# Kernel tuning notes

Hardware: AMD Instinct MI355X
Metric: run time of the kernel (lower is better)

Reference implementation:

```python
import jax, jax.numpy as jnp
import numpy as np

E, CAP, S, H, I, K = 160, 120, 3200, 2048, 192, 6  # experts, capacity, seq, hidden, per-device ffn dim, top-k


def setup_inputs() -> dict:
    key = jax.random.key(0)
    ks = jax.random.split(key, 8)
    hidden_states = jax.random.normal(ks[0], (S, H), jnp.float32)
    token_index = jax.random.randint(ks[1], (E, CAP), 0, S, dtype=jnp.int32)
    # re_index is a permutation mapping concatenated per-expert outputs back to (topk, seq) order
    re_index = jax.random.permutation(ks[2], E * CAP).astype(jnp.int32)
    topk_weight = jax.random.uniform(ks[3], (K, S, 1), jnp.float32)
    shared_out = jax.random.normal(ks[4], (1, S, H), jnp.float32)
    scale = 0.02
    gate_w = jax.random.normal(ks[5], (E, I, H), jnp.float32) * scale
    up_w = jax.random.normal(ks[6], (E, I, H), jnp.float32) * scale
    down_w = jax.random.normal(ks[7], (E, H, I), jnp.float32) * scale
    return {
        "hidden_states": hidden_states,
        "token_index": token_index,
        "re_index": re_index,
        "topk_weight": topk_weight,
        "shared_out": shared_out,
        "gate_w": gate_w,
        "up_w": up_w,
        "down_w": down_w,
    }


def reference(hidden_states, token_index, re_index, topk_weight, shared_out, gate_w, up_w, down_w):
    # Gather per-expert token groups: [E, CAP, H]
    x = hidden_states[token_index]
    # SwiGLU expert FFN, batched over all experts (grouped GEMM)
    g = jnp.einsum('ech,eih->eci', x, gate_w)   # [E, CAP, I]
    u = jnp.einsum('ech,eih->eci', x, up_w)     # [E, CAP, I]
    h = jax.nn.silu(g) * u
    o = jnp.einsum('eci,ehi->ech', h, down_w)   # [E, CAP, H]
    # Scatter back into (topk, seq) layout and combine with routing weights
    flat = o.reshape(E * CAP, H)[re_index].reshape(K, S, H)
    out = (flat * topk_weight).sum(axis=0, keepdims=True) + shared_out  # [1, S, H]
    return out
```

## Files before the change

### kernel.cpp

```cpp
#include <hip/hip_runtime.h>
#include <hip/hip_bf16.h>

#define E_ 160
#define CAP_ 120
#define S_ 3200
#define H_ 2048
#define I_ 192
#define K_ 6
#define MP_ 128

typedef __attribute__((ext_vector_type(8))) short short8;
typedef __attribute__((ext_vector_type(4))) float f32x4;

__device__ __forceinline__ unsigned pack2bf(float a, float b) {
  return __builtin_amdgcn_perm(__float_as_uint(b), __float_as_uint(a), 0x07060302u);
}
__device__ __forceinline__ short f2bf1(float a) {
  return (short)(__float_as_uint(a) >> 16);
}
__device__ __forceinline__ float bf2f(short s) {
  return __uint_as_float(((unsigned)(unsigned short)s) << 16);
}

__global__ __launch_bounds__(256) void k_gather(
    const float* __restrict__ hidden, const int* __restrict__ tok,
    short* __restrict__ xb)
{
  int b = blockIdx.x;
  int e = b >> 7, c = b & 127;
  int col = threadIdx.x * 8;
  short* dst = xb + (size_t)b * H_ + col;
  if (c < CAP_) {
    int row = tok[e * CAP_ + c];
    const float* src = hidden + (size_t)row * H_ + col;
    float4 f0 = *(const float4*)src;
    float4 f1 = *(const float4*)(src + 4);
    int4 v;
    v.x = (int)pack2bf(f0.x, f0.y); v.y = (int)pack2bf(f0.z, f0.w);
    v.z = (int)pack2bf(f1.x, f1.y); v.w = (int)pack2bf(f1.z, f1.w);
    *(int4*)dst = v;
  } else {
    *(int4*)dst = make_int4(0, 0, 0, 0);
  }
}

__global__ __launch_bounds__(256) void k_gateup(
    const short* __restrict__ xb, const float* __restrict__ gw,
    const float* __restrict__ uw, short* __restrict__ hb)
{
  __shared__ __align__(16) char smem[34816];
  short* As = (short*)smem;
  short* Bs = As + 128 * 64;

  int bid = blockIdx.x;
  int e = bid / 3, t = bid - e * 3;
  int i0 = t * 64;
  int tid = threadIdx.x;
  int lane = tid & 63, w = tid >> 6;
  int wr = w >> 1, wc = w & 1;
  int lrow = lane & 15, lq = lane >> 4;

  f32x4 acc[4][4] = {};
  const size_t xbase = (size_t)e * MP_ * H_;

  for (int kk = 0; kk < H_ / 64; ++kk) {
    int k0 = kk * 64;
#pragma unroll
    for (int r = 0; r < 4; ++r) {
      int q = r * 256 + tid;
      int row = q >> 3, cc = q & 7;
      int4 v = *(const int4*)(xb + xbase + (size_t)row * H_ + k0 + cc * 8);
      *(int4*)(As + row * 64 + cc * 8) = v;
    }
#pragma unroll
    for (int r = 0; r < 8; ++r) {
      int p = r * 256 + tid;
      int row = p >> 4, cc = p & 15;
      const float* srcw = (row < 64)
          ? (gw + ((size_t)e * I_ + i0 + row) * H_ + k0 + cc * 4)
          : (uw + ((size_t)e * I_ + i0 + row - 64) * H_ + k0 + cc * 4);
      float4 f = *(const float4*)srcw;
      uint2 pv;
      pv.x = pack2bf(f.x, f.y); pv.y = pack2bf(f.z, f.w);
      *(uint2*)(Bs + row * 64 + cc * 4) = pv;
    }
    __syncthreads();
#pragma unroll
    for (int ks = 0; ks < 2; ++ks) {
      int koff = ks * 32 + lq * 8;
      short8 a[4], bb[4];
#pragma unroll
      for (int tr = 0; tr < 4; ++tr)
        a[tr] = *(const short8*)(As + (wr * 64 + tr * 16 + lrow) * 64 + koff);
#pragma unroll
      for (int tc = 0; tc < 4; ++tc)
        bb[tc] = *(const short8*)(Bs + (wc * 64 + tc * 16 + lrow) * 64 + koff);
#pragma unroll
      for (int tr = 0; tr < 4; ++tr)
#pragma unroll
        for (int tc = 0; tc < 4; ++tc)
          acc[tr][tc] = __builtin_amdgcn_mfma_f32_16x16x32_bf16(
              a[tr], bb[tc], acc[tr][tc], 0, 0, 0);
    }
    __syncthreads();
  }

  float* exch = (float*)smem;
  if (wc == 0) {
#pragma unroll
    for (int tr = 0; tr < 4; ++tr)
#pragma unroll
      for (int tc = 0; tc < 4; ++tc)
#pragma unroll
        for (int rg = 0; rg < 4; ++rg) {
          int lr = tr * 16 + lq * 4 + rg;
          int lcol = tc * 16 + lrow;
          exch[(wr * 64 + lr) * 68 + lcol] = acc[tr][tc][rg];
        }
  }
  __syncthreads();
  if (wc == 1) {
#pragma unroll
    for (int tr = 0; tr < 4; ++tr)
#pragma unroll
      for (int tc = 0; tc < 4; ++tc)
#pragma unroll
        for (int rg = 0; rg < 4; ++rg) {
          int lr = tr * 16 + lq * 4 + rg;
          int lcol = tc * 16 + lrow;
          float g = exch[(wr * 64 + lr) * 68 + lcol];
          float u = acc[tr][tc][rg];
          float hv = g / (1.f + __expf(-g)) * u;
          hb[((size_t)e * MP_ + wr * 64 + lr) * I_ + i0 + lcol] = f2bf1(hv);
        }
  }
}

__global__ __launch_bounds__(256) void k_down(
    const short* __restrict__ hb, const float* __restrict__ dw,
    short* __restrict__ ob)
{
  __shared__ __align__(16) short As[128 * 64];
  __shared__ __align__(16) short Bs[128 * 64];
  int bid = blockIdx.x;
  int e = bid >> 4, t = bid & 15;
  int n0 = t * 128;
  int tid = threadIdx.x;
  int lane = tid & 63, w = tid >> 6;
  int wr = w >> 1, wc = w & 1;
  int lrow = lane & 15, lq = lane >> 4;

  f32x4 acc[4][4] = {};

  for (int kk = 0; kk < 3; ++kk) {
    int k0 = kk * 64;
#pragma unroll
    for (int r = 0; r < 4; ++r) {
      int q = r * 256 + tid;
      int row = q >> 3, cc = q & 7;
      int4 v = *(const int4*)(hb + ((size_t)e * MP_ + row) * I_ + k0 + cc * 8);
      *(int4*)(As + row * 64 + cc * 8) = v;
    }
#pragma unroll
    for (int r = 0; r < 8; ++r) {
      int p = r * 256 + tid;
      int row = p >> 4, cc = p & 15;
      const float* srcw = dw + ((size_t)e * H_ + n0 + row) * I_ + k0 + cc * 4;
      float4 f = *(const float4*)srcw;
      uint2 pv;
      pv.x = pack2bf(f.x, f.y); pv.y = pack2bf(f.z, f.w);
      *(uint2*)(Bs + row * 64 + cc * 4) = pv;
    }
    __syncthreads();
#pragma unroll
    for (int ks = 0; ks < 2; ++ks) {
      int koff = ks * 32 + lq * 8;
      short8 a[4], bb[4];
#pragma unroll
      for (int tr = 0; tr < 4; ++tr)
        a[tr] = *(const short8*)(As + (wr * 64 + tr * 16 + lrow) * 64 + koff);
#pragma unroll
      for (int tc = 0; tc < 4; ++tc)
        bb[tc] = *(const short8*)(Bs + (wc * 64 + tc * 16 + lrow) * 64 + koff);
#pragma unroll
      for (int tr = 0; tr < 4; ++tr)
#pragma unroll
        for (int tc = 0; tc < 4; ++tc)
          acc[tr][tc] = __builtin_amdgcn_mfma_f32_16x16x32_bf16(
              a[tr], bb[tc], acc[tr][tc], 0, 0, 0);
    }
    __syncthreads();
  }

#pragma unroll
  for (int tr = 0; tr < 4; ++tr) {
#pragma unroll
    for (int rg = 0; rg < 4; ++rg) {
      int c = wr * 64 + tr * 16 + lq * 4 + rg;
      if (c < CAP_) {
#pragma unroll
        for (int tc = 0; tc < 4; ++tc) {
          int col = n0 + wc * 64 + tc * 16 + lrow;
          ob[((size_t)e * CAP_ + c) * H_ + col] = f2bf1(acc[tr][tc][rg]);
        }
      }
    }
  }
}

__global__ __launch_bounds__(256) void k_combine(
    const short* __restrict__ ob, const int* __restrict__ re_index,
    const float* __restrict__ topk, const float* __restrict__ shared_out,
    float* __restrict__ out)
{
  int s = blockIdx.x;
  int c0 = threadIdx.x * 8;
  const float* sh = shared_out + (size_t)s * H_ + c0;
  float4 s0 = *(const float4*)sh;
  float4 s1 = *(const float4*)(sh + 4);
  float r[8] = {s0.x, s0.y, s0.z, s0.w, s1.x, s1.y, s1.z, s1.w};
#pragma unroll
  for (int k = 0; k < K_; ++k) {
    int p = k * S_ + s;
    int idx = re_index[p];
    float wgt = topk[p];
    const short* row = ob + (size_t)idx * H_ + c0;
    short8 v = *(const short8*)row;
#pragma unroll
    for (int j = 0; j < 8; ++j) r[j] += wgt * bf2f(v[j]);
  }
  float* o = out + (size_t)s * H_ + c0;
  float4 o0, o1;
  o0.x = r[0]; o0.y = r[1]; o0.z = r[2]; o0.w = r[3];
  o1.x = r[4]; o1.y = r[5]; o1.z = r[6]; o1.w = r[7];
  *(float4*)o = o0;
  *(float4*)(o + 4) = o1;
}

extern "C" void kernel_launch(void* const* d_in, const int* in_sizes, int n_in,
                              void* d_out, int out_size, void* d_ws, size_t ws_size,
                              hipStream_t stream) {
  const float* hidden     = (const float*)d_in[0];
  const int*   tok        = (const int*)d_in[1];
  const int*   re_index   = (const int*)d_in[2];
  const float* topk       = (const float*)d_in[3];
  const float* shared_out = (const float*)d_in[4];
  const float* gw         = (const float*)d_in[5];
  const float* uw         = (const float*)d_in[6];
  const float* dw         = (const float*)d_in[7];
  float* out = (float*)d_out;

  char* ws = (char*)d_ws;
  short* xb = (short*)ws;
  short* hb = (short*)(ws + (size_t)E_ * MP_ * H_ * 2);
  short* ob = (short*)(ws + (size_t)E_ * MP_ * H_ * 2
                          + (size_t)E_ * MP_ * I_ * 2);

  hipLaunchKernelGGL(k_gather,  dim3(E_ * MP_), dim3(256), 0, stream, hidden, tok, xb);
  hipLaunchKernelGGL(k_gateup,  dim3(E_ * 3),   dim3(256), 0, stream, xb, gw, uw, hb);
  hipLaunchKernelGGL(k_down,    dim3(E_ * 16),  dim3(256), 0, stream, hb, dw, ob);
  hipLaunchKernelGGL(k_combine, dim3(S_),       dim3(256), 0, stream, ob, re_index, topk, shared_out, out);
}
```

Measured before the change: 755.5 us.

## Fuse token gather into gate/up GEMM with register prefetch and swizzled LDS

Removes the separate gather kernel and loads hidden rows directly by token index inside the gate/up GEMM, converting to bf16 on the fly. The gate/up main loop now double-buffers LDS with register prefetch of the next K slice, using one barrier per iteration and raised wave priority around the MFMAs. Both GEMMs use an XOR-swizzled LDS layout to cut bank conflicts and remap block IDs so neighbouring blocks land on the same XCD. This saves the intermediate bf16 activation round trip through memory. In exchange it adds register pressure, and the gate/up kernel now requests 64KB of shared memory with a launch bound of 2 blocks per CU.

New measurement: 706.7 us. -6.5%, faster.

```diff
diff --git a/kernel.cpp b/kernel.cpp
--- a/kernel.cpp
+++ b/kernel.cpp
@@ -21,89 +21,112 @@
 __device__ __forceinline__ float bf2f(short s) {
   return __uint_as_float(((unsigned)(unsigned short)s) << 16);
 }
-
-__global__ __launch_bounds__(256) void k_gather(
+__device__ __forceinline__ int swz(int row, int inrow_byte) {
+  return row * 128 + (inrow_byte ^ ((row & 7) << 4));
+}
+
+__global__ __launch_bounds__(256, 2) void k_gateup(
     const float* __restrict__ hidden, const int* __restrict__ tok,
-    short* __restrict__ xb)
+    const float* __restrict__ gw, const float* __restrict__ uw,
+    short* __restrict__ hb)
 {
-  int b = blockIdx.x;
-  int e = b >> 7, c = b & 127;
-  int col = threadIdx.x * 8;
-  short* dst = xb + (size_t)b * H_ + col;
-  if (c < CAP_) {
-    int row = tok[e * CAP_ + c];
-    const float* src = hidden + (size_t)row * H_ + col;
-    float4 f0 = *(const float4*)src;
-    float4 f1 = *(const float4*)(src + 4);
-    int4 v;
-    v.x = (int)pack2bf(f0.x, f0.y); v.y = (int)pack2bf(f0.z, f0.w);
-    v.z = (int)pack2bf(f1.x, f1.y); v.w = (int)pack2bf(f1.z, f1.w);
-    *(int4*)dst = v;
-  } else {
-    *(int4*)dst = make_int4(0, 0, 0, 0);
-  }
-}
-
-__global__ __launch_bounds__(256) void k_gateup(
-    const short* __restrict__ xb, const float* __restrict__ gw,
-    const float* __restrict__ uw, short* __restrict__ hb)
-{
-  __shared__ __align__(16) char smem[34816];
-  short* As = (short*)smem;
-  short* Bs = As + 128 * 64;
+  __shared__ __align__(16) char smem[65536];
 
   int bid = blockIdx.x;
-  int e = bid / 3, t = bid - e * 3;
+  int lb = (bid & 7) * 60 + (bid >> 3);
+  int e = lb / 3, t = lb - e * 3;
   int i0 = t * 64;
   int tid = threadIdx.x;
   int lane = tid & 63, w = tid >> 6;
   int wr = w >> 1, wc = w & 1;
   int lrow = lane & 15, lq = lane >> 4;
 
+  int rr = tid >> 3;
+  int cq = tid & 7;
+
+  int aoff[4];
+  int arowok[4];
+#pragma unroll
+  for (int c = 0; c < 4; ++c) {
+    int row = rr + 32 * c;
+    int ok = (row < CAP_);
+    int tk = ok ? tok[e * CAP_ + row] : 0;
+    aoff[c] = tk * H_ + cq * 8;
+    arowok[c] = ok;
+  }
+  int boff[4];
+#pragma unroll
+  for (int c = 0; c < 4; ++c) {
+    int row = rr + 32 * c;
+    int wrow = (c < 2) ? row : row - 64;
+    boff[c] = (e * I_ + i0 + wrow) * H_ + cq * 8;
+  }
+
   f32x4 acc[4][4] = {};
-  const size_t xbase = (size_t)e * MP_ * H_;
+  float4 av[4][2], bv[4][2];
+
+  auto gload = [&](int k0) {
+#pragma unroll
+    for (int c = 0; c < 4; ++c) {
+      const float* ap = hidden + aoff[c] + k0;
+      av[c][0] = *(const float4*)ap;
+      av[c][1] = *(const float4*)(ap + 4);
+      const float* bp = ((c < 2) ? gw : uw) + boff[c] + k0;
+      bv[c][0] = *(const float4*)bp;
+      bv[c][1] = *(const float4*)(bp + 4);
+    }
+  };
+
+  gload(0);
 
   for (int kk = 0; kk < H_ / 64; ++kk) {
-    int k0 = kk * 64;
-#pragma unroll
-    for (int r = 0; r < 4; ++r) {
-      int q = r * 256 + tid;
-      int row = q >> 3, cc = q & 7;
-      int4 v = *(const int4*)(xb + xbase + (size_t)row * H_ + k0 + cc * 8);
-      *(int4*)(As + row * 64 + cc * 8) = v;
-    }
-#pragma unroll
-    for (int r = 0; r < 8; ++r) {
-      int p = r * 256 + tid;
-      int row = p >> 4, cc = p & 15;
-      const float* srcw = (row < 64)
-          ? (gw + ((size_t)e * I_ + i0 + row) * H_ + k0 + cc * 4)
-          : (uw + ((size_t)e * I_ + i0 + row - 64) * H_ + k0 + cc * 4);
-      float4 f = *(const float4*)srcw;
-      uint2 pv;
-      pv.x = pack2bf(f.x, f.y); pv.y = pack2bf(f.z, f.w);
-      *(uint2*)(Bs + row * 64 + cc * 4) = pv;
-    }
-    __syncthreads();
+    char* As = smem + ((kk & 1) << 15);
+    char* Bs = As + 16384;
+#pragma unroll
+    for (int c = 0; c < 4; ++c) {
+      int row = rr + 32 * c;
+      int4 va;
+      va.x = (int)pack2bf(av[c][0].x, av[c][0].y);
+      va.y = (int)pack2bf(av[c][0].z, av[c][0].w);
+      va.z = (int)pack2bf(av[c][1].x, av[c][1].y);
+      va.w = (int)pack2bf(av[c][1].z, av[c][1].w);
+      if (!arowok[c]) va = make_int4(0, 0, 0, 0);
+      *(int4*)(As + swz(row, cq * 16)) = va;
+      int4 vb;
+      vb.x = (int)pack2bf(bv[c][0].x, bv[c][0].y);
+      vb.y = (int)pack2bf(bv[c][0].z, bv[c][0].w);
+      vb.z = (int)pack2bf(bv[c][1].x, bv[c][1].y);
+      vb.w = (int)pack2bf(bv[c][1].z, bv[c][1].w);
+      *(int4*)(Bs + swz(row, cq * 16)) = vb;
+    }
+    if (kk + 1 < H_ / 64) gload((kk + 1) * 64);
+    __builtin_amdgcn_sched_barrier(0);
+    asm volatile("s_waitcnt lgkmcnt(0)" ::: "memory");
+    __builtin_amdgcn_s_barrier();
 #pragma unroll
     for (int ks = 0; ks < 2; ++ks) {
-      int koff = ks * 32 + lq * 8;
       short8 a[4], bb[4];
 #pragma unroll
-      for (int tr = 0; tr < 4; ++tr)
-        a[tr] = *(const short8*)(As + (wr * 64 + tr * 16 + lrow) * 64 + koff);
-#pragma unroll
-      for (int tc = 0; tc < 4; ++tc)
-        bb[tc] = *(const short8*)(Bs + (wc * 64 + tc * 16 + lrow) * 64 + koff);
+      for (int tr = 0; tr < 4; ++tr) {
+        int row = wr * 64 + tr * 16 + lrow;
+        a[tr] = *(const short8*)(As + swz(row, ks * 64 + lq * 16));
+      }
+#pragma unroll
+      for (int tc = 0; tc < 4; ++tc) {
+        int row = wc * 64 + tc * 16 + lrow;
+        bb[tc] = *(const short8*)(Bs + swz(row, ks * 64 + lq * 16));
+      }
+      __builtin_amdgcn_s_setprio(1);
 #pragma unroll
       for (int tr = 0; tr < 4; ++tr)
 #pragma unroll
         for (int tc = 0; tc < 4; ++tc)
           acc[tr][tc] = __builtin_amdgcn_mfma_f32_16x16x32_bf16(
               a[tr], bb[tc], acc[tr][tc], 0, 0, 0);
-    }
-    __syncthreads();
-  }
+      __builtin_amdgcn_s_setprio(0);
+    }
+  }
+  __syncthreads();
 
   float* exch = (float*)smem;
   if (wc == 0) {
@@ -140,10 +163,12 @@
     const short* __restrict__ hb, const float* __restrict__ dw,
     short* __restrict__ ob)
 {
-  __shared__ __align__(16) short As[128 * 64];
-  __shared__ __align__(16) short Bs[128 * 64];
+  __shared__ __align__(16) char smem2[32768];
+  char* As = smem2;
+  char* Bs = smem2 + 16384;
   int bid = blockIdx.x;
-  int e = bid >> 4, t = bid & 15;
+  int lb = (bid & 7) * 320 + (bid >> 3);
+  int e = lb >> 4, t = lb & 15;
   int n0 = t * 128;
   int tid = threadIdx.x;
   int lane = tid & 63, w = tid >> 6;
@@ -159,7 +184,7 @@
       int q = r * 256 + tid;
       int row = q >> 3, cc = q & 7;
       int4 v = *(const int4*)(hb + ((size_t)e * MP_ + row) * I_ + k0 + cc * 8);
-      *(int4*)(As + row * 64 + cc * 8) = v;
+      *(int4*)(As + swz(row, cc * 16)) = v;
     }
 #pragma unroll
     for (int r = 0; r < 8; ++r) {
@@ -169,19 +194,22 @@
       float4 f = *(const float4*)srcw;
       uint2 pv;
       pv.x = pack2bf(f.x, f.y); pv.y = pack2bf(f.z, f.w);
-      *(uint2*)(Bs + row * 64 + cc * 4) = pv;
+      *(uint2*)(Bs + swz(row, cc * 8)) = pv;
     }
     __syncthreads();
 #pragma unroll
     for (int ks = 0; ks < 2; ++ks) {
-      int koff = ks * 32 + lq * 8;
       short8 a[4], bb[4];
 #pragma unroll
-      for (int tr = 0; tr < 4; ++tr)
-        a[tr] = *(const short8*)(As + (wr * 64 + tr * 16 + lrow) * 64 + koff);
-#pragma unroll
-      for (int tc = 0; tc < 4; ++tc)
-        bb[tc] = *(const short8*)(Bs + (wc * 64 + tc * 16 + lrow) * 64 + koff);
+      for (int tr = 0; tr < 4; ++tr) {
+        int row = wr * 64 + tr * 16 + lrow;
+        a[tr] = *(const short8*)(As + swz(row, ks * 64 + lq * 16));
+      }
+#pragma unroll
+      for (int tc = 0; tc < 4; ++tc) {
+        int row = wc * 64 + tc * 16 + lrow;
+        bb[tc] = *(const short8*)(Bs + swz(row, ks * 64 + lq * 16));
+      }
 #pragma unroll
       for (int tr = 0; tr < 4; ++tr)
 #pragma unroll
@@ -251,13 +279,10 @@
   float* out = (float*)d_out;
 
   char* ws = (char*)d_ws;
-  short* xb = (short*)ws;
-  short* hb = (short*)(ws + (size_t)E_ * MP_ * H_ * 2);
-  short* ob = (short*)(ws + (size_t)E_ * MP_ * H_ * 2
-                          + (size_t)E_ * MP_ * I_ * 2);
-
-  hipLaunchKernelGGL(k_gather,  dim3(E_ * MP_), dim3(256), 0, stream, hidden, tok, xb);
-  hipLaunchKernelGGL(k_gateup,  dim3(E_ * 3),   dim3(256), 0, stream, xb, gw, uw, hb);
-  hipLaunchKernelGGL(k_down,    dim3(E_ * 16),  dim3(256), 0, stream, hb, dw, ob);
-  hipLaunchKernelGGL(k_combine, dim3(S_),       dim3(256), 0, stream, ob, re_index, topk, shared_out, out);
-}
+  short* hb = (short*)ws;
+  short* ob = (short*)(ws + (size_t)E_ * MP_ * I_ * 2);
+
+  hipLaunchKernelGGL(k_gateup,  dim3(E_ * 3),  dim3(256), 0, stream, hidden, tok, gw, uw, hb);
+  hipLaunchKernelGGL(k_down,    dim3(E_ * 16), dim3(256), 0, stream, hb, dw, ob);
+  hipLaunchKernelGGL(k_combine, dim3(S_),      dim3(256), 0, stream, ob, re_index, topk, shared_out, out);
+}
```
